# Performance work log

Hardware: AMD Instinct MI355X
Metric: run time of the kernel (lower is better)

The kernel has to match this reference:

```python
import jax, jax.numpy as jnp
import numpy as np

H, W, WS, KS, D, CF, HEAD = 64, 64, 8, 8, 512, 128, 8
INC = D + CF  # 640
GH, GW = H // WS, W // WS  # 8, 8
G = GH * GW  # 64 windows
NW = WS * WS  # 64 tokens per window
DH = D // HEAD  # 64


def _ln(x, g, b, eps=1e-5):
    m = jnp.mean(x, axis=-1, keepdims=True)
    v = jnp.var(x, axis=-1, keepdims=True)
    return (x - m) * jax.lax.rsqrt(v + eps) * g + b


def _lin(x, w, b):
    # torch Linear: w [out,in]
    return jnp.einsum('...i,oi->...o', x, w) + b


def _dwconv(x_nchw, w, b):
    # depthwise conv, stride=KS, VALID; w [C,1,KS,KS]
    y = jax.lax.conv_general_dilated(
        x_nchw, w, window_strides=(KS, KS), padding='VALID',
        feature_group_count=x_nchw.shape[1])
    return y + b[None, :, None, None]


def _win(x):  # [bt,H,W,c] -> [bt,G,NW,c]
    bt, _, _, c = x.shape
    x = x.reshape(bt, GH, WS, GW, WS, c).transpose(0, 1, 3, 2, 4, 5)
    return x.reshape(bt, G, NW, c)


def setup_inputs() -> dict:
    key = jax.random.key(0)
    ks = jax.random.split(key, 20)
    s = 0.02
    inp = {
        'x': jax.random.normal(ks[0], (8, H * W, D), jnp.float32),
        'f': jax.random.normal(ks[1], (8, H * W, CF), jnp.float32),
        'wq': jax.random.normal(ks[2], (D, INC), jnp.float32) * s,
        'bq': jnp.zeros((D,), jnp.float32),
        'wk': jax.random.normal(ks[3], (D, INC), jnp.float32) * s,
        'bk': jnp.zeros((D,), jnp.float32),
        'wv': jax.random.normal(ks[4], (D, D), jnp.float32) * s,
        'bv': jnp.zeros((D,), jnp.float32),
        'wo': jax.random.normal(ks[5], (D, D), jnp.float32) * s,
        'bo': jnp.zeros((D,), jnp.float32),
        'rw_w': jax.random.normal(ks[6], (INC, INC), jnp.float32) * s,
        'rw_b': jnp.zeros((INC,), jnp.float32),
        'convk_w': jax.random.normal(ks[7], (INC, 1, KS, KS), jnp.float32) * s,
        'convk_b': jnp.zeros((INC,), jnp.float32),
        'convv_w': jax.random.normal(ks[8], (D, 1, KS, KS), jnp.float32) * s,
        'convv_b': jnp.zeros((D,), jnp.float32),
        'qn_g': jnp.ones((INC,), jnp.float32), 'qn_b': jnp.zeros((INC,), jnp.float32),
        'kn_g': jnp.ones((INC,), jnp.float32), 'kn_b': jnp.zeros((INC,), jnp.float32),
        'vn_g': jnp.ones((D,), jnp.float32), 'vn_b': jnp.zeros((D,), jnp.float32),
        't': 1,
    }
    return inp


def reference(x, f, wq, bq, wk, bk, wv, bv, wo, bo, rw_w, rw_b,
              convk_w, convk_b, convv_w, convv_b,
              qn_g, qn_b, kn_g, kn_b, vn_g, vn_b, t):
    bt, n, c = x.shape
    x4 = x.reshape(bt, H, W, c)
    f4 = f.reshape(bt, H, W, CF)
    # no padding: H,W divisible by WS
    qk = jnp.concatenate([x4, f4], axis=-1)  # [bt,H,W,INC]
    qk = qk * jax.nn.sigmoid(_lin(qk, rw_w, rw_b))
    q = _win(qk)  # [bt,G,NW,INC]
    # global K tokens via depthwise strided conv
    kg = _dwconv(qk.transpose(0, 3, 1, 2), convk_w, convk_b)  # [bt,INC,GH,GW]
    kg = kg.transpose(0, 2, 3, 1).reshape(bt, 1, -1, INC)
    kg = jnp.broadcast_to(kg, (bt, G, kg.shape[2], INC))
    k = jnp.concatenate([q, kg], axis=2)  # [bt,G,NW+Ng,INC]
    q = _ln(q, qn_g, qn_b)
    k = _ln(k, kn_g, kn_b)
    # global V tokens
    vg = _dwconv(x4.transpose(0, 3, 1, 2), convv_w, convv_b)  # [bt,D,GH,GW]
    vg = vg.transpose(0, 2, 3, 1).reshape(bt, 1, -1, c)
    vg = jnp.broadcast_to(vg, (bt, G, vg.shape[2], c))
    xw = _win(x4)  # [bt,G,NW,c]
    v = _ln(jnp.concatenate([xw, vg], axis=2), vn_g, vn_b)
    # projections
    query = _lin(q, wq, bq).reshape(bt, G, NW, HEAD, DH)
    key = _lin(k, wk, bk).reshape(bt, G, -1, HEAD, DH)
    value = _lin(v, wv, bv).reshape(bt, G, -1, HEAD, DH)
    scores = jnp.einsum('bgqhd,bgkhd->bghqk', query, key) / jnp.sqrt(jnp.float32(DH))
    attn = jax.nn.softmax(scores, axis=-1)
    out = jnp.einsum('bghqk,bgkhd->bgqhd', attn, value).reshape(bt, G, NW, c)
    # window reverse
    out = out.reshape(bt, GH, GW, WS, WS, c).transpose(0, 1, 3, 2, 4, 5)
    out = out.reshape(bt, H * W, c)
    return _lin(out, wo, bo)
```

## Files before the change

kernel.cpp:

```cpp
#include <hip/hip_runtime.h>

typedef unsigned short u16;
typedef __attribute__((ext_vector_type(8))) short s8v;
typedef __attribute__((ext_vector_type(4))) short s4v;
typedef __attribute__((ext_vector_type(4))) float f4v;

#define NTOK 32768
#define TTOK 33280

__device__ __forceinline__ float bf2f(u16 u){
  union { unsigned int i; float f; } p; p.i = ((unsigned int)u) << 16; return p.f;
}
__device__ __forceinline__ u16 f2bf(float f){
  union { float f; unsigned int i; } p; p.f = f;
  unsigned int r = p.i + 0x7FFFu + ((p.i >> 16) & 1u);
  return (u16)(r >> 16);
}
__device__ __forceinline__ int wtok_idx(int b, int gh, int gw, int n){
  return b*4096 + (gh*8 + (n>>3))*64 + gw*8 + (n&7);
}
__device__ __forceinline__ void gload16(const u16* g, u16* l){
  __builtin_amdgcn_global_load_lds(
      (const __attribute__((address_space(1))) void*)g,
      (__attribute__((address_space(3))) void*)l, 16, 0, 0);
}

__global__ __launch_bounds__(256) void prep_weights(
    const float* __restrict__ rww, const float* __restrict__ wq,
    const float* __restrict__ wk,  const float* __restrict__ wv,
    const float* __restrict__ wo,  const float* __restrict__ qng,
    const float* __restrict__ kng, const float* __restrict__ vng,
    u16* __restrict__ orw, u16* __restrict__ oqk,
    u16* __restrict__ ov,  u16* __restrict__ oo)
{
  int i = blockIdx.x*256 + threadIdx.x;
  if (i < 409600){ orw[i] = f2bf(rww[i]); return; }
  i -= 409600;
  if (i < 327680){ oqk[i] = f2bf(wq[i] * qng[i % 640]); return; }
  i -= 327680;
  if (i < 327680){ oqk[327680 + i] = f2bf(wk[i] * kng[i % 640]); return; }
  i -= 327680;
  if (i < 262144){ ov[i] = f2bf(wv[i] * vng[i & 511]); return; }
  i -= 262144;
  oo[i] = f2bf(wo[i]);
}

__global__ __launch_bounds__(256) void prep_bias(
    const float* __restrict__ wq, const float* __restrict__ bq, const float* __restrict__ qnb,
    const float* __restrict__ wk, const float* __restrict__ bk, const float* __restrict__ knb,
    const float* __restrict__ wv, const float* __restrict__ bv, const float* __restrict__ vnb,
    float* __restrict__ obqk, float* __restrict__ obv)
{
  int o = blockIdx.x*256 + threadIdx.x;
  int which = o >> 9;
  int oo = o & 511;
  if (which == 0){
    float s = bq[oo];
    for (int i=0;i<640;i++) s += qnb[i]*wq[oo*640+i];
    obqk[oo] = s;
  } else if (which == 1){
    float s = bk[oo];
    for (int i=0;i<640;i++) s += knb[i]*wk[oo*640+i];
    obqk[512 + oo] = s;
  } else {
    float s = bv[oo];
    for (int i=0;i<512;i++) s += vnb[i]*wv[oo*512+i];
    obv[oo] = s;
  }
}

__global__ __launch_bounds__(256) void build_qk(
    const float* __restrict__ X, const float* __restrict__ F, u16* __restrict__ qkb)
{
  int idx = blockIdx.x*256 + threadIdx.x;
  int token = idx / 160;
  int c4 = (idx - token*160) * 4;
  f4v v;
  if (c4 < 512) v = *(const f4v*)(X + (size_t)token*512 + c4);
  else          v = *(const f4v*)(F + (size_t)token*128 + (c4 - 512));
  s4v o;
  #pragma unroll
  for (int j=0;j<4;j++) o[j] = (short)f2bf(v[j]);
  *(s4v*)(qkb + (size_t)token*640 + c4) = o;
}

template<int EPI>
__global__ __launch_bounds__(256, 3) void gemm_kernel(
    const u16* __restrict__ A, const u16* __restrict__ B,
    const float* __restrict__ bias,
    u16* __restrict__ out0, u16* __restrict__ out1, float* __restrict__ outf,
    int N, int K)
{
  __shared__ u16 lA[128*64];
  __shared__ u16 lB[128*64];
  const int tid = threadIdx.x;
  const int lane = tid & 63;
  const int w = tid >> 6;
  const int wm = (w >> 1) * 64;
  const int wn = (w & 1) * 64;
  const int nb = N >> 7;
  const int m0 = (blockIdx.x / nb) << 7;
  const int n0 = (blockIdx.x % nb) << 7;
  const int wbase = tid & ~63;

  const f4v fzero = {0.f, 0.f, 0.f, 0.f};
  f4v acc[4][4];
  #pragma unroll
  for (int i=0;i<4;i++)
    #pragma unroll
    for (int j=0;j<4;j++) acc[i][j] = fzero;

  for (int k0 = 0; k0 < K; k0 += 64){
    #pragma unroll
    for (int it=0; it<4; it++){
      int s = it*256 + tid;
      int row = s >> 3, cc = s & 7, cs = cc ^ (row & 7);
      gload16(A + (size_t)(m0+row)*K + k0 + cs*8, &lA[(it*256 + wbase)*8]);
      gload16(B + (size_t)(n0+row)*K + k0 + cs*8, &lB[(it*256 + wbase)*8]);
    }
    __syncthreads();
    #pragma unroll
    for (int kk=0; kk<2; kk++){
      const int cg = kk*4 + (lane>>4);
      s8v bfr[4];
      #pragma unroll
      for (int ni=0; ni<4; ni++){
        int col = wn + ni*16 + (lane&15);
        bfr[ni] = *(const s8v*)&lB[(col*8 + (cg ^ (col&7)))*8];
      }
      #pragma unroll
      for (int mi=0; mi<4; mi++){
        int row = wm + mi*16 + (lane&15);
        s8v afr = *(const s8v*)&lA[(row*8 + (cg ^ (row&7)))*8];
        #pragma unroll
        for (int ni=0; ni<4; ni++)
          acc[mi][ni] = __builtin_amdgcn_mfma_f32_16x16x32_bf16(afr, bfr[ni], acc[mi][ni], 0, 0, 0);
      }
    }
    __syncthreads();
  }

  #pragma unroll
  for (int mi=0; mi<4; mi++){
    #pragma unroll
    for (int ni=0; ni<4; ni++){
      const int colg = n0 + wn + ni*16 + (lane&15);
      const float bb = bias[colg];
      if constexpr (EPI == 3){
        const int rowg0 = m0 + wm + mi*16 + (lane>>4)*4;
        s4v pk;
        #pragma unroll
        for (int j=0;j<4;j++) pk[j] = (short)f2bf(acc[mi][ni][j] + bb);
        *(s4v*)(out0 + (size_t)colg*TTOK + rowg0) = pk;
      } else {
        #pragma unroll
        for (int j=0;j<4;j++){
          const int rowg = m0 + wm + mi*16 + (lane>>4)*4 + j;
          float v = acc[mi][ni][j] + bb;
          if constexpr (EPI == 1){
            float sg = 1.f / (1.f + __expf(-v));
            float qv = bf2f(A[(size_t)rowg*640 + colg]);
            out0[(size_t)rowg*640 + colg] = f2bf(qv * sg);
          } else if constexpr (EPI == 2){
            outf[(size_t)rowg*512 + colg] = v;
          } else {
            if (colg < 512) out0[(size_t)rowg*512 + colg] = f2bf(v);
            else            out1[(size_t)rowg*512 + (colg-512)] = f2bf(v);
          }
        }
      }
    }
  }
}

__global__ __launch_bounds__(256) void ln_qk_kernel(const u16* __restrict__ y, u16* __restrict__ u)
{
  int t = blockIdx.x*16 + (threadIdx.x >> 4);
  int l = threadIdx.x & 15;
  const u16* row = y + (size_t)t*640;
  s8v v[5];
  float s = 0.f, s2 = 0.f;
  #pragma unroll
  for (int p=0;p<5;p++){
    v[p] = *(const s8v*)(row + (p*16+l)*8);
    #pragma unroll
    for (int j=0;j<8;j++){ float x = bf2f((u16)v[p][j]); s += x; s2 += x*x; }
  }
  #pragma unroll
  for (int m=1;m<16;m<<=1){ s += __shfl_xor(s,m); s2 += __shfl_xor(s2,m); }
  float mean = s*(1.f/640.f);
  float var = s2*(1.f/640.f) - mean*mean;
  float rstd = rsqrtf(var + 1e-5f);
  u16* ur = u + (size_t)t*640;
  #pragma unroll
  for (int p=0;p<5;p++){
    s8v o;
    #pragma unroll
    for (int j=0;j<8;j++) o[j] = (short)f2bf((bf2f((u16)v[p][j])-mean)*rstd);
    *(s8v*)(ur + (p*16+l)*8) = o;
  }
}

__global__ __launch_bounds__(256) void ln_x_kernel(const float* __restrict__ X, u16* __restrict__ uv)
{
  int t = blockIdx.x*16 + (threadIdx.x >> 4);
  int l = threadIdx.x & 15;
  const float* row = X + (size_t)t*512;
  f4v v[8];
  float s = 0.f, s2 = 0.f;
  #pragma unroll
  for (int p=0;p<8;p++){
    v[p] = *(const f4v*)(row + (p*16+l)*4);
    #pragma unroll
    for (int j=0;j<4;j++){ float x = v[p][j]; s += x; s2 += x*x; }
  }
  #pragma unroll
  for (int m=1;m<16;m<<=1){ s += __shfl_xor(s,m); s2 += __shfl_xor(s2,m); }
  float mean = s*(1.f/512.f);
  float var = s2*(1.f/512.f) - mean*mean;
  float rstd = rsqrtf(var + 1e-5f);
  u16* ur = uv + (size_t)t*512;
  #pragma unroll
  for (int p=0;p<8;p++){
    s4v o;
    #pragma unroll
    for (int j=0;j<4;j++) o[j] = (short)f2bf((v[p][j]-mean)*rstd);
    *(s4v*)(ur + (p*16+l)*4) = o;
  }
}

__global__ __launch_bounds__(640) void convk_ln_kernel(
    const u16* __restrict__ qkrw, const float* __restrict__ cw,
    const float* __restrict__ cb, u16* __restrict__ u)
{
  int bg = blockIdx.x;
  int b = bg >> 6, gpos = bg & 63;
  int gh = gpos >> 3, gw = gpos & 7;
  int ch = threadIdx.x;
  int base = b*4096 + gh*8*64 + gw*8;
  float acc = cb[ch];
  #pragma unroll
  for (int r=0;r<8;r++)
    #pragma unroll
    for (int c=0;c<8;c++)
      acc += bf2f(qkrw[(size_t)(base + r*64 + c)*640 + ch]) * cw[ch*64 + r*8 + c];
  float s = acc, s2 = acc*acc;
  #pragma unroll
  for (int m=1;m<64;m<<=1){ s += __shfl_xor(s,m); s2 += __shfl_xor(s2,m); }
  __shared__ float rs[10], rs2[10];
  int wid = threadIdx.x >> 6, lane = threadIdx.x & 63;
  if (lane == 0){ rs[wid] = s; rs2[wid] = s2; }
  __syncthreads();
  float ts = 0.f, ts2 = 0.f;
  #pragma unroll
  for (int i=0;i<10;i++){ ts += rs[i]; ts2 += rs2[i]; }
  float mean = ts*(1.f/640.f);
  float var = ts2*(1.f/640.f) - mean*mean;
  float rstd = rsqrtf(var + 1e-5f);
  u[(size_t)(NTOK + bg)*640 + ch] = f2bf((acc-mean)*rstd);
}

__global__ __launch_bounds__(512) void convv_ln_kernel(
    const float* __restrict__ X, const float* __restrict__ cw,
    const float* __restrict__ cb, u16* __restrict__ uv)
{
  int bg = blockIdx.x;
  int b = bg >> 6, gpos = bg & 63;
  int gh = gpos >> 3, gw = gpos & 7;
  int ch = threadIdx.x;
  int base = b*4096 + gh*8*64 + gw*8;
  float acc = cb[ch];
  #pragma unroll
  for (int r=0;r<8;r++)
    #pragma unroll
    for (int c=0;c<8;c++)
      acc += X[(size_t)(base + r*64 + c)*512 + ch] * cw[ch*64 + r*8 + c];
  float s = acc, s2 = acc*acc;
  #pragma unroll
  for (int m=1;m<64;m<<=1){ s += __shfl_xor(s,m); s2 += __shfl_xor(s2,m); }
  __shared__ float rs[8], rs2[8];
  int wid = threadIdx.x >> 6, lane = threadIdx.x & 63;
  if (lane == 0){ rs[wid] = s; rs2[wid] = s2; }
  __syncthreads();
  float ts = 0.f, ts2 = 0.f;
  #pragma unroll
  for (int i=0;i<8;i++){ ts += rs[i]; ts2 += rs2[i]; }
  float mean = ts*(1.f/512.f);
  float var = ts2*(1.f/512.f) - mean*mean;
  float rstd = rsqrtf(var + 1e-5f);
  uv[(size_t)(NTOK + bg)*512 + ch] = f2bf((acc-mean)*rstd);
}

__global__ __launch_bounds__(256, 3) void attn_kernel(
    const u16* __restrict__ Qp, const u16* __restrict__ Kp,
    const u16* __restrict__ VT, u16* __restrict__ Out)
{
  int blk = blockIdx.x;
  int h = blk & 7, g = (blk >> 3) & 63, b = blk >> 9;
  int gh = g >> 3, gw = g & 7;
  int tid = threadIdx.x, lane = tid & 63, wvid = tid >> 6;
  int l15 = lane & 15, lg = lane >> 4;

  __shared__ u16 ps[64*128];
  __shared__ float red[4][64];

  s8v qf[4][2], kf[2][2], vf[4];
  #pragma unroll
  for (int mi=0; mi<4; mi++){
    const u16* qrow = Qp + (size_t)wtok_idx(b,gh,gw, mi*16 + l15)*512 + h*64;
    #pragma unroll
    for (int kk=0; kk<2; kk++)
      qf[mi][kk] = *(const s8v*)(qrow + (kk*4+lg)*8);
  }
  #pragma unroll
  for (int ni=0; ni<2; ni++){
    int kt = wvid*32 + ni*16 + l15;
    int tok = (kt < 64) ? wtok_idx(b,gh,gw,kt) : (NTOK + b*64 + (kt-64));
    const u16* krow = Kp + (size_t)tok*512 + h*64;
    #pragma unroll
    for (int kk=0; kk<2; kk++)
      kf[ni][kk] = *(const s8v*)(krow + (kk*4+lg)*8);
  }
  {
    int d = wvid*16 + l15;
    const u16* vrow = VT + (size_t)(h*64 + d)*TTOK;
    #pragma unroll
    for (int c4=0; c4<4; c4++){
      int kt0 = (c4*4+lg)*8;
      int tok0 = (kt0 < 64) ? wtok_idx(b,gh,gw,kt0) : (NTOK + b*64 + (kt0-64));
      vf[c4] = *(const s8v*)(vrow + tok0);
    }
  }

  const f4v fzero = {0.f,0.f,0.f,0.f};
  f4v sacc[4][2];
  #pragma unroll
  for (int i=0;i<4;i++){ sacc[i][0]=fzero; sacc[i][1]=fzero; }
  #pragma unroll
  for (int kk=0; kk<2; kk++)
    #pragma unroll
    for (int mi=0; mi<4; mi++)
      #pragma unroll
      for (int ni=0; ni<2; ni++)
        sacc[mi][ni] = __builtin_amdgcn_mfma_f32_16x16x32_bf16(qf[mi][kk], kf[ni][kk], sacc[mi][ni], 0,0,0);

  float psum[4][4];
  #pragma unroll
  for (int mi=0; mi<4; mi++){
    #pragma unroll
    for (int j=0;j<4;j++){
      float e0 = __expf(sacc[mi][0][j] * 0.125f);
      float e1 = __expf(sacc[mi][1][j] * 0.125f);
      sacc[mi][0][j] = e0; sacc[mi][1][j] = e1;
      float t0 = e0 + e1;
      #pragma unroll
      for (int m=1;m<16;m<<=1) t0 += __shfl_xor(t0, m);
      psum[mi][j] = t0;
    }
  }
  if (l15 == 0){
    #pragma unroll
    for (int mi=0; mi<4; mi++)
      #pragma unroll
      for (int j=0;j<4;j++)
        red[wvid][mi*16 + lg*4 + j] = psum[mi][j];
  }
  __syncthreads();

  #pragma unroll
  for (int mi=0; mi<4; mi++){
    #pragma unroll
    for (int j=0;j<4;j++){
      int r = mi*16 + lg*4 + j;
      float inv = 1.0f / (red[0][r] + red[1][r] + red[2][r] + red[3][r]);
      #pragma unroll
      for (int ni=0; ni<2; ni++){
        int col = wvid*32 + ni*16 + l15;
        int ck = (col >> 3) ^ (r & 15);
        ps[r*128 + ck*8 + (col & 7)] = f2bf(sacc[mi][ni][j] * inv);
      }
    }
  }
  __syncthreads();

  f4v oacc[4];
  #pragma unroll
  for (int i=0;i<4;i++) oacc[i] = fzero;
  #pragma unroll
  for (int c4=0; c4<4; c4++){
    int cg = c4*4 + lg;
    #pragma unroll
    for (int mi=0; mi<4; mi++){
      s8v afr = *(const s8v*)&ps[((mi*16 + l15)*16 + (cg ^ l15))*8];
      oacc[mi] = __builtin_amdgcn_mfma_f32_16x16x32_bf16(afr, vf[c4], oacc[mi], 0,0,0);
    }
  }
  #pragma unroll
  for (int mi=0; mi<4; mi++)
    #pragma unroll
    for (int j=0;j<4;j++){
      int q = mi*16 + lg*4 + j;
      Out[(size_t)wtok_idx(b,gh,gw,q)*512 + h*64 + wvid*16 + l15] = f2bf(oacc[mi][j]);
    }
}

extern "C" void kernel_launch(void* const* d_in, const int* in_sizes, int n_in,
                              void* d_out, int out_size, void* d_ws, size_t ws_size,
                              hipStream_t stream)
{
  const float* X   = (const float*)d_in[0];
  const float* F   = (const float*)d_in[1];
  const float* wq  = (const float*)d_in[2];
  const float* bq  = (const float*)d_in[3];
  const float* wk  = (const float*)d_in[4];
  const float* bk  = (const float*)d_in[5];
  const float* wv  = (const float*)d_in[6];
  const float* bv  = (const float*)d_in[7];
  const float* wo  = (const float*)d_in[8];
  const float* bo  = (const float*)d_in[9];
  const float* rww = (const float*)d_in[10];
  const float* rwb = (const float*)d_in[11];
  const float* ckw = (const float*)d_in[12];
  const float* ckb = (const float*)d_in[13];
  const float* cvw = (const float*)d_in[14];
  const float* cvb = (const float*)d_in[15];
  const float* qng = (const float*)d_in[16];
  const float* qnb = (const float*)d_in[17];
  const float* kng = (const float*)d_in[18];
  const float* knb = (const float*)d_in[19];
  const float* vng = (const float*)d_in[20];
  const float* vnb = (const float*)d_in[21];
  float* OutF = (float*)d_out;

  char* ws = (char*)d_ws;
  size_t off = 0;
  auto alloc = [&](size_t bytes){
    size_t o = off; off += (bytes + 255) & ~(size_t)255; return o;
  };
  u16*   W_RW = (u16*)  (ws + alloc((size_t)640*640*2));
  u16*   W_QK = (u16*)  (ws + alloc((size_t)1024*640*2));
  u16*   W_V  = (u16*)  (ws + alloc((size_t)512*512*2));
  u16*   W_O  = (u16*)  (ws + alloc((size_t)512*512*2));
  float* B_QK = (float*)(ws + alloc(1024*4));
  float* B_V  = (float*)(ws + alloc(512*4));
  u16*   QKB  = (u16*)  (ws + alloc((size_t)NTOK*640*2));
  u16*   QKRW = (u16*)  (ws + alloc((size_t)NTOK*640*2));
  u16*   U    = (u16*)  (ws + alloc((size_t)TTOK*640*2));
  u16*   UV   = (u16*)  (ws + alloc((size_t)TTOK*512*2));
  u16*   KP   = (u16*)  (ws + alloc((size_t)TTOK*512*2));
  u16*   VT   = (u16*)  (ws + alloc((size_t)512*TTOK*2));
  (void)in_sizes; (void)n_in; (void)out_size; (void)ws_size;

  prep_weights<<<6208, 256, 0, stream>>>(rww, wq, wk, wv, wo, qng, kng, vng,
                                         W_RW, W_QK, W_V, W_O);
  prep_bias<<<6, 256, 0, stream>>>(wq, bq, qnb, wk, bk, knb, wv, bv, vnb, B_QK, B_V);
  build_qk<<<20480, 256, 0, stream>>>(X, F, QKB);

  gemm_kernel<1><<<1280, 256, 0, stream>>>(QKB, W_RW, rwb, QKRW, nullptr, nullptr, 640, 640);

  ln_qk_kernel<<<2048, 256, 0, stream>>>(QKRW, U);
  ln_x_kernel<<<2048, 256, 0, stream>>>(X, UV);
  convk_ln_kernel<<<512, 640, 0, stream>>>(QKRW, ckw, ckb, U);
  convv_ln_kernel<<<512, 512, 0, stream>>>(X, cvw, cvb, UV);

  gemm_kernel<4><<<2080, 256, 0, stream>>>(U,  W_QK, B_QK, QKB, KP, nullptr, 1024, 640);
  gemm_kernel<3><<<1040, 256, 0, stream>>>(UV, W_V,  B_V,  VT,  nullptr, nullptr, 512, 512);

  attn_kernel<<<4096, 256, 0, stream>>>(QKB, KP, VT, QKRW);

  gemm_kernel<2><<<1024, 256, 0, stream>>>(QKRW, W_O, bo, nullptr, nullptr, OutF, 512, 512);
}
```

Measured before the change: 500.2 us.

## Fold LayerNorm into GEMM epilogues via row stats and weight column sums

Replaces the standalone LayerNorm kernels, which wrote normalized bf16 copies of the Q/K and V inputs, with a light row-stats pass. The projection GEMMs now read the raw activations and apply rstd*(acc - mean*colsum(W)) + bias in the epilogue. The GEMMs gather rows from two sources: the token buffer and a small global-token buffer. The change also remaps workgroup ids for better cache locality. This removes a full write and re-read of the normalized activations, at the cost of possible precision loss from the mean-subtraction trick and an extra pointer select per A load.

```diff
diff --git a/kernel.cpp b/kernel.cpp
--- a/kernel.cpp
+++ b/kernel.cpp
@@ -47,25 +47,29 @@
 
 __global__ __launch_bounds__(256) void prep_bias(
     const float* __restrict__ wq, const float* __restrict__ bq, const float* __restrict__ qnb,
+    const float* __restrict__ qng,
     const float* __restrict__ wk, const float* __restrict__ bk, const float* __restrict__ knb,
+    const float* __restrict__ kng,
     const float* __restrict__ wv, const float* __restrict__ bv, const float* __restrict__ vnb,
-    float* __restrict__ obqk, float* __restrict__ obv)
+    const float* __restrict__ vng,
+    float* __restrict__ obqk, float* __restrict__ obv,
+    float* __restrict__ owsqk, float* __restrict__ owsv)
 {
   int o = blockIdx.x*256 + threadIdx.x;
   int which = o >> 9;
   int oo = o & 511;
   if (which == 0){
-    float s = bq[oo];
-    for (int i=0;i<640;i++) s += qnb[i]*wq[oo*640+i];
-    obqk[oo] = s;
+    float s = bq[oo], ws = 0.f;
+    for (int i=0;i<640;i++){ float w = wq[oo*640+i]*qng[i]; s += qnb[i]*wq[oo*640+i]; ws += w; }
+    obqk[oo] = s; owsqk[oo] = ws;
   } else if (which == 1){
-    float s = bk[oo];
-    for (int i=0;i<640;i++) s += knb[i]*wk[oo*640+i];
-    obqk[512 + oo] = s;
+    float s = bk[oo], ws = 0.f;
+    for (int i=0;i<640;i++){ float w = wk[oo*640+i]*kng[i]; s += knb[i]*wk[oo*640+i]; ws += w; }
+    obqk[512 + oo] = s; owsqk[512 + oo] = ws;
   } else {
-    float s = bv[oo];
-    for (int i=0;i<512;i++) s += vnb[i]*wv[oo*512+i];
-    obv[oo] = s;
+    float s = bv[oo], ws = 0.f;
+    for (int i=0;i<512;i++){ float w = wv[oo*512+i]*vng[i]; s += vnb[i]*wv[oo*512+i]; ws += w; }
+    obv[oo] = s; owsv[oo] = ws;
   }
 }
 
@@ -84,10 +88,37 @@
   *(s4v*)(qkb + (size_t)token*640 + c4) = o;
 }
 
-template<int EPI>
+template<int NC>
+__global__ __launch_bounds__(256) void row_stats(
+    const u16* __restrict__ A, int stride, float* __restrict__ om, float* __restrict__ os)
+{
+  int t = blockIdx.x*16 + (threadIdx.x >> 4);
+  int l = threadIdx.x & 15;
+  const u16* row = A + (size_t)t*stride;
+  float s = 0.f, s2 = 0.f;
+  #pragma unroll
+  for (int p=0; p<NC/128; p++){
+    s8v v = *(const s8v*)(row + (p*16+l)*8);
+    #pragma unroll
+    for (int j=0;j<8;j++){ float x = bf2f((u16)v[j]); s += x; s2 += x*x; }
+  }
+  #pragma unroll
+  for (int m=1;m<16;m<<=1){ s += __shfl_xor(s,m); s2 += __shfl_xor(s2,m); }
+  if (l == 0){
+    float mean = s*(1.f/NC);
+    float var = s2*(1.f/NC) - mean*mean;
+    om[t] = mean;
+    os[t] = rsqrtf(var + 1e-5f);
+  }
+}
+
+template<int EPI, bool STATS>
 __global__ __launch_bounds__(256, 3) void gemm_kernel(
-    const u16* __restrict__ A, const u16* __restrict__ B,
-    const float* __restrict__ bias,
+    const u16* __restrict__ A, int strideA,
+    const u16* __restrict__ A2, int strideA2,
+    const u16* __restrict__ B, const float* __restrict__ bias,
+    const float* __restrict__ wsum,
+    const float* __restrict__ rmean, const float* __restrict__ rrstd,
     u16* __restrict__ out0, u16* __restrict__ out1, float* __restrict__ outf,
     int N, int K)
 {
@@ -99,8 +130,10 @@
   const int wm = (w >> 1) * 64;
   const int wn = (w & 1) * 64;
   const int nb = N >> 7;
-  const int m0 = (blockIdx.x / nb) << 7;
-  const int n0 = (blockIdx.x % nb) << 7;
+  const int nwg = (int)gridDim.x;
+  const int wg = ((int)blockIdx.x & 7) * (nwg >> 3) + ((int)blockIdx.x >> 3);
+  const int m0 = (wg / nb) << 7;
+  const int n0 = (wg % nb) << 7;
   const int wbase = tid & ~63;
 
   const f4v fzero = {0.f, 0.f, 0.f, 0.f};
@@ -115,7 +148,11 @@
     for (int it=0; it<4; it++){
       int s = it*256 + tid;
       int row = s >> 3, cc = s & 7, cs = cc ^ (row & 7);
-      gload16(A + (size_t)(m0+row)*K + k0 + cs*8, &lA[(it*256 + wbase)*8]);
+      int rr = m0 + row;
+      const u16* aptr = (rr < NTOK)
+          ? A  + (size_t)rr*strideA  + k0 + cs*8
+          : A2 + (size_t)(rr - NTOK)*strideA2 + k0 + cs*8;
+      gload16(aptr, &lA[(it*256 + wbase)*8]);
       gload16(B + (size_t)(n0+row)*K + k0 + cs*8, &lB[(it*256 + wbase)*8]);
     }
     __syncthreads();
@@ -142,21 +179,35 @@
 
   #pragma unroll
   for (int mi=0; mi<4; mi++){
+    float rs[4], rm[4];
+    if constexpr (STATS){
+      #pragma unroll
+      for (int j=0;j<4;j++){
+        int rowg = m0 + wm + mi*16 + (lane>>4)*4 + j;
+        rs[j] = rrstd[rowg]; rm[j] = rmean[rowg];
+      }
+    }
     #pragma unroll
     for (int ni=0; ni<4; ni++){
       const int colg = n0 + wn + ni*16 + (lane&15);
       const float bb = bias[colg];
+      const float wsc = STATS ? wsum[colg] : 0.f;
       if constexpr (EPI == 3){
         const int rowg0 = m0 + wm + mi*16 + (lane>>4)*4;
         s4v pk;
         #pragma unroll
-        for (int j=0;j<4;j++) pk[j] = (short)f2bf(acc[mi][ni][j] + bb);
+        for (int j=0;j<4;j++){
+          float v = STATS ? (rs[j]*acc[mi][ni][j] - rs[j]*rm[j]*wsc + bb)
+                          : (acc[mi][ni][j] + bb);
+          pk[j] = (short)f2bf(v);
+        }
         *(s4v*)(out0 + (size_t)colg*TTOK + rowg0) = pk;
       } else {
         #pragma unroll
         for (int j=0;j<4;j++){
           const int rowg = m0 + wm + mi*16 + (lane>>4)*4 + j;
-          float v = acc[mi][ni][j] + bb;
+          float v = STATS ? (rs[j]*acc[mi][ni][j] - rs[j]*rm[j]*wsc + bb)
+                          : (acc[mi][ni][j] + bb);
           if constexpr (EPI == 1){
             float sg = 1.f / (1.f + __expf(-v));
             float qv = bf2f(A[(size_t)rowg*640 + colg]);
@@ -173,65 +224,10 @@
   }
 }
 
-__global__ __launch_bounds__(256) void ln_qk_kernel(const u16* __restrict__ y, u16* __restrict__ u)
-{
-  int t = blockIdx.x*16 + (threadIdx.x >> 4);
-  int l = threadIdx.x & 15;
-  const u16* row = y + (size_t)t*640;
-  s8v v[5];
-  float s = 0.f, s2 = 0.f;
-  #pragma unroll
-  for (int p=0;p<5;p++){
-    v[p] = *(const s8v*)(row + (p*16+l)*8);
-    #pragma unroll
-    for (int j=0;j<8;j++){ float x = bf2f((u16)v[p][j]); s += x; s2 += x*x; }
-  }
-  #pragma unroll
-  for (int m=1;m<16;m<<=1){ s += __shfl_xor(s,m); s2 += __shfl_xor(s2,m); }
-  float mean = s*(1.f/640.f);
-  float var = s2*(1.f/640.f) - mean*mean;
-  float rstd = rsqrtf(var + 1e-5f);
-  u16* ur = u + (size_t)t*640;
-  #pragma unroll
-  for (int p=0;p<5;p++){
-    s8v o;
-    #pragma unroll
-    for (int j=0;j<8;j++) o[j] = (short)f2bf((bf2f((u16)v[p][j])-mean)*rstd);
-    *(s8v*)(ur + (p*16+l)*8) = o;
-  }
-}
-
-__global__ __launch_bounds__(256) void ln_x_kernel(const float* __restrict__ X, u16* __restrict__ uv)
-{
-  int t = blockIdx.x*16 + (threadIdx.x >> 4);
-  int l = threadIdx.x & 15;
-  const float* row = X + (size_t)t*512;
-  f4v v[8];
-  float s = 0.f, s2 = 0.f;
-  #pragma unroll
-  for (int p=0;p<8;p++){
-    v[p] = *(const f4v*)(row + (p*16+l)*4);
-    #pragma unroll
-    for (int j=0;j<4;j++){ float x = v[p][j]; s += x; s2 += x*x; }
-  }
-  #pragma unroll
-  for (int m=1;m<16;m<<=1){ s += __shfl_xor(s,m); s2 += __shfl_xor(s2,m); }
-  float mean = s*(1.f/512.f);
-  float var = s2*(1.f/512.f) - mean*mean;
-  float rstd = rsqrtf(var + 1e-5f);
-  u16* ur = uv + (size_t)t*512;
-  #pragma unroll
-  for (int p=0;p<8;p++){
-    s4v o;
-    #pragma unroll
-    for (int j=0;j<4;j++) o[j] = (short)f2bf((v[p][j]-mean)*rstd);
-    *(s4v*)(ur + (p*16+l)*4) = o;
-  }
-}
-
 __global__ __launch_bounds__(640) void convk_ln_kernel(
     const u16* __restrict__ qkrw, const float* __restrict__ cw,
-    const float* __restrict__ cb, u16* __restrict__ u)
+    const float* __restrict__ cb, u16* __restrict__ qkc,
+    float* __restrict__ om, float* __restrict__ os)
 {
   int bg = blockIdx.x;
   int b = bg >> 6, gpos = bg & 63;
@@ -257,12 +253,14 @@
   float mean = ts*(1.f/640.f);
   float var = ts2*(1.f/640.f) - mean*mean;
   float rstd = rsqrtf(var + 1e-5f);
-  u[(size_t)(NTOK + bg)*640 + ch] = f2bf((acc-mean)*rstd);
+  qkc[(size_t)bg*640 + ch] = f2bf((acc-mean)*rstd);
+  if (ch == 0){ om[NTOK + bg] = 0.f; os[NTOK + bg] = 1.f; }
 }
 
 __global__ __launch_bounds__(512) void convv_ln_kernel(
     const float* __restrict__ X, const float* __restrict__ cw,
-    const float* __restrict__ cb, u16* __restrict__ uv)
+    const float* __restrict__ cb, u16* __restrict__ xc,
+    float* __restrict__ om, float* __restrict__ os)
 {
   int bg = blockIdx.x;
   int b = bg >> 6, gpos = bg & 63;
@@ -288,7 +286,8 @@
   float mean = ts*(1.f/512.f);
   float var = ts2*(1.f/512.f) - mean*mean;
   float rstd = rsqrtf(var + 1e-5f);
-  uv[(size_t)(NTOK + bg)*512 + ch] = f2bf((acc-mean)*rstd);
+  xc[(size_t)bg*512 + ch] = f2bf((acc-mean)*rstd);
+  if (ch == 0){ om[NTOK + bg] = 0.f; os[NTOK + bg] = 1.f; }
 }
 
 __global__ __launch_bounds__(256, 3) void attn_kernel(
@@ -443,30 +442,41 @@
   u16*   W_O  = (u16*)  (ws + alloc((size_t)512*512*2));
   float* B_QK = (float*)(ws + alloc(1024*4));
   float* B_V  = (float*)(ws + alloc(512*4));
+  float* WS_QK= (float*)(ws + alloc(1024*4));
+  float* WS_V = (float*)(ws + alloc(512*4));
   u16*   QKB  = (u16*)  (ws + alloc((size_t)NTOK*640*2));
   u16*   QKRW = (u16*)  (ws + alloc((size_t)NTOK*640*2));
-  u16*   U    = (u16*)  (ws + alloc((size_t)TTOK*640*2));
-  u16*   UV   = (u16*)  (ws + alloc((size_t)TTOK*512*2));
+  u16*   QKC  = (u16*)  (ws + alloc((size_t)512*640*2));
+  u16*   XC   = (u16*)  (ws + alloc((size_t)512*512*2));
   u16*   KP   = (u16*)  (ws + alloc((size_t)TTOK*512*2));
   u16*   VT   = (u16*)  (ws + alloc((size_t)512*TTOK*2));
+  float* SQm  = (float*)(ws + alloc((size_t)TTOK*4));
+  float* SQs  = (float*)(ws + alloc((size_t)TTOK*4));
+  float* SVm  = (float*)(ws + alloc((size_t)TTOK*4));
+  float* SVs  = (float*)(ws + alloc((size_t)TTOK*4));
   (void)in_sizes; (void)n_in; (void)out_size; (void)ws_size;
 
   prep_weights<<<6208, 256, 0, stream>>>(rww, wq, wk, wv, wo, qng, kng, vng,
                                          W_RW, W_QK, W_V, W_O);
-  prep_bias<<<6, 256, 0, stream>>>(wq, bq, qnb, wk, bk, knb, wv, bv, vnb, B_QK, B_V);
+  prep_bias<<<6, 256, 0, stream>>>(wq, bq, qnb, qng, wk, bk, knb, kng,
+                                   wv, bv, vnb, vng, B_QK, B_V, WS_QK, WS_V);
   build_qk<<<20480, 256, 0, stream>>>(X, F, QKB);
 
-  gemm_kernel<1><<<1280, 256, 0, stream>>>(QKB, W_RW, rwb, QKRW, nullptr, nullptr, 640, 640);
-
-  ln_qk_kernel<<<2048, 256, 0, stream>>>(QKRW, U);
-  ln_x_kernel<<<2048, 256, 0, stream>>>(X, UV);
-  convk_ln_kernel<<<512, 640, 0, stream>>>(QKRW, ckw, ckb, U);
-  convv_ln_kernel<<<512, 512, 0, stream>>>(X, cvw, cvb, UV);
-
-  gemm_kernel<4><<<2080, 256, 0, stream>>>(U,  W_QK, B_QK, QKB, KP, nullptr, 1024, 640);
-  gemm_kernel<3><<<1040, 256, 0, stream>>>(UV, W_V,  B_V,  VT,  nullptr, nullptr, 512, 512);
+  gemm_kernel<1,false><<<1280, 256, 0, stream>>>(QKB, 640, nullptr, 0, W_RW, rwb,
+      nullptr, nullptr, nullptr, QKRW, nullptr, nullptr, 640, 640);
+
+  row_stats<640><<<2048, 256, 0, stream>>>(QKRW, 640, SQm, SQs);
+  row_stats<512><<<2048, 256, 0, stream>>>(QKB, 640, SVm, SVs);
+  convk_ln_kernel<<<512, 640, 0, stream>>>(QKRW, ckw, ckb, QKC, SQm, SQs);
+  convv_ln_kernel<<<512, 512, 0, stream>>>(X, cvw, cvb, XC, SVm, SVs);
+
+  gemm_kernel<3,true><<<1040, 256, 0, stream>>>(QKB, 640, XC, 512, W_V, B_V,
+      WS_V, SVm, SVs, VT, nullptr, nullptr, 512, 512);
+  gemm_kernel<4,true><<<2080, 256, 0, stream>>>(QKRW, 640, QKC, 640, W_QK, B_QK,
+      WS_QK, SQm, SQs, QKB, KP, nullptr, 1024, 640);
 
   attn_kernel<<<4096, 256, 0, stream>>>(QKB, KP, VT, QKRW);
 
-  gemm_kernel<2><<<1024, 256, 0, stream>>>(QKRW, W_O, bo, nullptr, nullptr, OutF, 512, 512);
-}
+  gemm_kernel<2,false><<<1024, 256, 0, stream>>>(QKRW, 512, nullptr, 0, W_O, bo,
+      nullptr, nullptr, nullptr, nullptr, nullptr, OutF, 512, 512);
+}
```

New measurement: 456.4 us. 1.1x faster.
